# Performance work log

Measured on AMD Instinct MI355X. Metric: run time of the kernel, lower is better.

The kernel has to match this reference:

```python
import jax, jax.numpy as jnp
import numpy as np

EPS = 1e-6
L, H, D, DFF = 4, 6, 6, 64  # n_layers, num_heads(=dim, head_dim=1), d_hid, ffn hidden


def layernorm(x, w, b):
    mu = jnp.mean(x, axis=-1, keepdims=True)
    var = jnp.mean((x - mu) ** 2, axis=-1, keepdims=True)
    return (x - mu) / jnp.sqrt(var + EPS) * w + b


def autocorr(x, qw, qb, kw, kb, vw, vb, l1w, l1b):
    # x: [B,S,H]; head_dim==1 so per-head Linear is scalar w*x+b per head.
    k_in = jnp.concatenate([x[:, :1], x[:, :-1]], axis=1)   # roll right, first row kept
    v_in = jnp.concatenate([x[:, 1:], x[:, -1:]], axis=1)   # roll left, last row kept
    q = x * qw + qb
    k = k_in * kw + kb
    v = v_in * vw + vb
    teo = q * q - k * v                                      # [B,S,H]
    # nn.LayerNorm([1]) over size-1 axis: mean==x, var==0 -> output is bias
    normed = (teo - teo) / jnp.sqrt(EPS) * l1w + l1b
    scores = jax.nn.softmax(normed, axis=1)                  # over seq dim
    return scores * teo


def mha(x, p, li, ai):
    out = autocorr(x, p['qw'][li, ai], p['qb'][li, ai], p['kw'][li, ai],
                   p['kb'][li, ai], p['vw'][li, ai], p['vb'][li, ai],
                   p['ln1_w'][li, ai], p['ln1_b'][li, ai])
    return layernorm(out + x, p['mha_ln_w'][li, ai], p['mha_ln_b'][li, ai])


def setup_inputs() -> dict:
    key = jax.random.key(0)
    ks = jax.random.split(key, 24)
    n = jax.random.normal
    inp = {
        'x_batch': n(ks[0], (128, 4096, 6), jnp.float32),
        'enc_output': n(ks[1], (128, 4096, 6), jnp.float32),
        'dec_ln_w': jnp.ones((D,), jnp.float32),
        'dec_ln_b': jnp.zeros((D,), jnp.float32),
        'qw': n(ks[2], (L, 2, H), jnp.float32),
        'qb': n(ks[3], (L, 2, H), jnp.float32) * 0.1,
        'kw': n(ks[4], (L, 2, H), jnp.float32),
        'kb': n(ks[5], (L, 2, H), jnp.float32) * 0.1,
        'vw': n(ks[6], (L, 2, H), jnp.float32),
        'vb': n(ks[7], (L, 2, H), jnp.float32) * 0.1,
        'ln1_w': jnp.ones((L, 2), jnp.float32),
        'ln1_b': jnp.zeros((L, 2), jnp.float32),
        'mha_ln_w': jnp.ones((L, 2, D), jnp.float32),
        'mha_ln_b': jnp.zeros((L, 2, D), jnp.float32),
        'ffn_w1': n(ks[8], (L, DFF, D), jnp.float32) * (1.0 / np.sqrt(D)),
        'ffn_b1': jnp.zeros((L, DFF), jnp.float32),
        'ffn_w2': n(ks[9], (L, D, DFF), jnp.float32) * (1.0 / np.sqrt(DFF)),
        'ffn_b2': jnp.zeros((L, D), jnp.float32),
        'ffn_ln_w': jnp.ones((L, D), jnp.float32),
        'ffn_ln_b': jnp.zeros((L, D), jnp.float32),
    }
    return inp


def reference(x_batch, enc_output, dec_ln_w, dec_ln_b, qw, qb, kw, kb, vw, vb,
              ln1_w, ln1_b, mha_ln_w, mha_ln_b, ffn_w1, ffn_b1, ffn_w2, ffn_b2,
              ffn_ln_w, ffn_ln_b):
    p = dict(qw=qw, qb=qb, kw=kw, kb=kb, vw=vw, vb=vb, ln1_w=ln1_w, ln1_b=ln1_b,
             mha_ln_w=mha_ln_w, mha_ln_b=mha_ln_b)
    x = layernorm(x_batch, dec_ln_w, dec_ln_b)  # dropout p=0 -> identity
    for li in range(L):
        x = mha(x, p, li, 0)   # self-attention block
        x = mha(x, p, li, 1)   # "enc" attention block (also self, per source)
        h = jax.nn.relu(jnp.einsum('bsd,fd->bsf', x, ffn_w1[li]) + ffn_b1[li])
        y = jnp.einsum('bsf,df->bsd', h, ffn_w2[li]) + ffn_b2[li] + x
        x = layernorm(y, ffn_ln_w[li], ffn_ln_b[li])
    return x
```

## Files before the change

### kernel.cpp

```cpp
#include <hip/hip_runtime.h>

#define S_LEN  4096
#define DM     6
#define NLAYER 4
#define NFF    64
#define HALO   8
#define TPB    256
#define OUT_PER_WAVE 112
#define BLK_X 10

typedef float    vf2 __attribute__((ext_vector_type(2)));
typedef _Float16 vh2 __attribute__((ext_vector_type(2)));

#define REC    13
#define FPAIRS (NFF/2)
#define PACK_TOTAL (NLAYER*FPAIRS*REC)

__device__ __forceinline__ vf2 splat2(float s){ vf2 r; r.x = s; r.y = s; return r; }
__device__ __forceinline__ vh2 bch2(unsigned u){ return __builtin_bit_cast(vh2, u); }

__device__ __forceinline__ unsigned pack2(float lo, float hi){
    _Float16 a = (_Float16)lo, b = (_Float16)hi;
    unsigned short ua = __builtin_bit_cast(unsigned short, a);
    unsigned short ub = __builtin_bit_cast(unsigned short, b);
    return (unsigned)ua | ((unsigned)ub << 16);
}

__global__ void prep_weights(const float* __restrict__ w1,
                             const float* __restrict__ b1,
                             const float* __restrict__ w2,
                             unsigned* __restrict__ ws) {
    int i = blockIdx.x * 256 + threadIdx.x;
    if (i >= PACK_TOTAL) return;
    int li = i / (FPAIRS*REC);
    int r  = i % (FPAIRS*REC);
    int fp = r / REC;
    int j  = r % REC;
    float lo, hi;
    if (j < 6) {
        lo = w1[li*NFF*DM + (2*fp)*DM + j];
        hi = w1[li*NFF*DM + (2*fp+1)*DM + j];
    } else if (j < 12) {
        int d = j - 6;
        lo = w2[li*DM*NFF + d*NFF + 2*fp];
        hi = w2[li*DM*NFF + d*NFF + 2*fp + 1];
    } else {
        lo = b1[li*NFF + 2*fp];
        hi = b1[li*NFF + 2*fp + 1];
    }
    ws[i] = pack2(lo, hi);
}

__device__ __forceinline__ void ln6v(vf2* v, const float* __restrict__ w,
                                     const float* __restrict__ b) {
    vf2 mu = (((v[0]+v[1])+(v[2]+v[3]))+(v[4]+v[5])) * (1.0f/6.0f);
    vf2 var = splat2(0.0f);
#pragma unroll
    for (int d = 0; d < DM; ++d) { vf2 dd = v[d]-mu; var = __builtin_elementwise_fma(dd, dd, var); }
    vf2 a = var * (1.0f/6.0f) + splat2(1e-6f);
    vf2 r; r.x = rsqrtf(a.x); r.y = rsqrtf(a.y);
#pragma unroll
    for (int d = 0; d < DM; ++d)
        v[d] = __builtin_elementwise_fma((v[d]-mu)*r, splat2(w[d]), splat2(b[d]));
}

__global__ __launch_bounds__(TPB)
void decoder_fused(const float* __restrict__ x_batch,
                   const float* __restrict__ dec_ln_w, const float* __restrict__ dec_ln_b,
                   const float* __restrict__ qw, const float* __restrict__ qb,
                   const float* __restrict__ kw, const float* __restrict__ kb,
                   const float* __restrict__ vw, const float* __restrict__ vb,
                   const float* __restrict__ mha_ln_w, const float* __restrict__ mha_ln_b,
                   const unsigned* __restrict__ wsp,
                   const float* __restrict__ ffn_b2,
                   const float* __restrict__ ffn_ln_w, const float* __restrict__ ffn_ln_b,
                   float* __restrict__ out) {
    const int lane = threadIdx.x & 63;
    const int w    = blockIdx.x * (TPB/64) + (threadIdx.x >> 6);
    const int b    = blockIdx.y;
    const int p    = w * OUT_PER_WAVE - HALO + 2*lane;

    vf2 x2[DM];
    if (p >= 0 && p + 1 < S_LEN) {
        const float4* s = reinterpret_cast<const float4*>(x_batch + ((size_t)b*S_LEN + p)*DM);
        float4 a0 = s[0], a1 = s[1], a2 = s[2];
        x2[0].x=a0.x; x2[1].x=a0.y; x2[2].x=a0.z; x2[3].x=a0.w; x2[4].x=a1.x; x2[5].x=a1.y;
        x2[0].y=a1.z; x2[1].y=a1.w; x2[2].y=a2.x; x2[3].y=a2.y; x2[4].y=a2.z; x2[5].y=a2.w;
    } else {
        const int pc = min(max(p, 0), S_LEN-1);
        const float2* s = reinterpret_cast<const float2*>(x_batch + ((size_t)b*S_LEN + pc)*DM);
        float2 a0 = s[0], a1 = s[1], a2 = s[2];
        x2[0] = splat2(a0.x); x2[1] = splat2(a0.y); x2[2] = splat2(a1.x);
        x2[3] = splat2(a1.y); x2[4] = splat2(a2.x); x2[5] = splat2(a2.y);
    }

    ln6v(x2, dec_ln_w, dec_ln_b);

#pragma unroll 1
    for (int li = 0; li < NLAYER; ++li) {
#pragma unroll 1
        for (int ai = 0; ai < 2; ++ai) {
            const int base = (li*2 + ai) * DM;
            vf2 xm[DM], xp[DM];
#pragma unroll
            for (int d = 0; d < DM; ++d) {
                float up = __shfl_up (x2[d].y, 1);
                float dn = __shfl_down(x2[d].x, 1);
                xm[d].x = (p <= 0) ? x2[d].x : up;
                xm[d].y = x2[d].x;
                xp[d].x = x2[d].y;
                xp[d].y = (p + 1 >= S_LEN - 1) ? x2[d].y : dn;
            }
#pragma unroll
            for (int d = 0; d < DM; ++d) {
                vf2 q = __builtin_elementwise_fma(x2[d], splat2(qw[base+d]), splat2(qb[base+d]));
                vf2 k = __builtin_elementwise_fma(xm[d], splat2(kw[base+d]), splat2(kb[base+d]));
                vf2 v = __builtin_elementwise_fma(xp[d], splat2(vw[base+d]), splat2(vb[base+d]));
                vf2 teo = __builtin_elementwise_fma(q, q, -(k*v));
                x2[d] = __builtin_elementwise_fma(teo, splat2(1.0f/(float)S_LEN), x2[d]);
            }
            ln6v(x2, mha_ln_w + base, mha_ln_b + base);
        }

        {
            const unsigned* wl = wsp + (size_t)li * FPAIRS * REC;
            const float*    b2 = ffn_b2 + li*DM;

            vh2 xdA[DM], xdB[DM];
#pragma unroll
            for (int d = 0; d < DM; ++d) {
                _Float16 ha = (_Float16)x2[d].x, hb = (_Float16)x2[d].y;
                xdA[d].x = ha; xdA[d].y = ha;
                xdB[d].x = hb; xdB[d].y = hb;
            }
            vh2 accA[DM], accB[DM];
#pragma unroll
            for (int d = 0; d < DM; ++d) { accA[d] = (vh2)(_Float16)0; accB[d] = (vh2)(_Float16)0; }

#pragma unroll 8
            for (int fp = 0; fp < FPAIRS; ++fp) {
                const unsigned* wp = wl + fp*REC;
                vh2 hA = bch2(wp[12]);
                vh2 hB = hA;
#pragma unroll
                for (int d = 0; d < DM; ++d) {
                    vh2 w1p = bch2(wp[d]);
                    hA = __builtin_elementwise_fma(xdA[d], w1p, hA);
                    hB = __builtin_elementwise_fma(xdB[d], w1p, hB);
                }
                vh2 z = (vh2)(_Float16)0;
                hA = __builtin_elementwise_max(hA, z);
                hB = __builtin_elementwise_max(hB, z);
#pragma unroll
                for (int d = 0; d < DM; ++d) {
                    vh2 w2p = bch2(wp[6+d]);
                    accA[d] = __builtin_elementwise_fma(hA, w2p, accA[d]);
                    accB[d] = __builtin_elementwise_fma(hB, w2p, accB[d]);
                }
            }
#pragma unroll
            for (int d = 0; d < DM; ++d) {
                x2[d].x = x2[d].x + b2[d] + ((float)accA[d].x + (float)accA[d].y);
                x2[d].y = x2[d].y + b2[d] + ((float)accB[d].x + (float)accB[d].y);
            }
            ln6v(x2, ffn_ln_w + li*DM, ffn_ln_b + li*DM);
        }
    }

    if (lane >= 4 && lane < 60 && p < S_LEN) {
        float4* dst = reinterpret_cast<float4*>(out + ((size_t)b*S_LEN + p)*DM);
        float4 a0, a1, a2;
        a0.x=x2[0].x; a0.y=x2[1].x; a0.z=x2[2].x; a0.w=x2[3].x;
        a1.x=x2[4].x; a1.y=x2[5].x; a1.z=x2[0].y; a1.w=x2[1].y;
        a2.x=x2[2].y; a2.y=x2[3].y; a2.z=x2[4].y; a2.w=x2[5].y;
        dst[0]=a0; dst[1]=a1; dst[2]=a2;
    }
}

extern "C" void kernel_launch(void* const* d_in, const int* in_sizes, int n_in,
                              void* d_out, int out_size, void* d_ws, size_t ws_size,
                              hipStream_t stream) {
    const float* x_batch  = (const float*)d_in[0];
    const float* dec_ln_w = (const float*)d_in[2];
    const float* dec_ln_b = (const float*)d_in[3];
    const float* qw       = (const float*)d_in[4];
    const float* qb       = (const float*)d_in[5];
    const float* kw       = (const float*)d_in[6];
    const float* kb       = (const float*)d_in[7];
    const float* vw       = (const float*)d_in[8];
    const float* vb       = (const float*)d_in[9];
    const float* mha_ln_w = (const float*)d_in[12];
    const float* mha_ln_b = (const float*)d_in[13];
    const float* ffn_w1   = (const float*)d_in[14];
    const float* ffn_b1   = (const float*)d_in[15];
    const float* ffn_w2   = (const float*)d_in[16];
    const float* ffn_b2   = (const float*)d_in[17];
    const float* ffn_ln_w = (const float*)d_in[18];
    const float* ffn_ln_b = (const float*)d_in[19];
    float* out = (float*)d_out;
    unsigned* wsp = (unsigned*)d_ws;

    prep_weights<<<(PACK_TOTAL + 255)/256, 256, 0, stream>>>(ffn_w1, ffn_b1, ffn_w2, wsp);

    const int B = in_sizes[0] / (S_LEN * DM);
    dim3 grid(BLK_X, B);
    decoder_fused<<<grid, TPB, 0, stream>>>(
        x_batch, dec_ln_w, dec_ln_b, qw, qb, kw, kb, vw, vb,
        mha_ln_w, mha_ln_b, wsp, ffn_b2, ffn_ln_w, ffn_ln_b, out);
}
```

Baseline: 155.2 us.

## Compute FFN with MFMA 16x16x16 f16 via per-wave LDS staging

```diff
diff --git a/kernel.cpp b/kernel.cpp
--- a/kernel.cpp
+++ b/kernel.cpp
@@ -10,15 +10,24 @@
 #define BLK_X 10
 
 typedef float    vf2 __attribute__((ext_vector_type(2)));
+typedef float    vf4 __attribute__((ext_vector_type(4)));
 typedef _Float16 vh2 __attribute__((ext_vector_type(2)));
-
-#define REC    13
-#define FPAIRS (NFF/2)
-#define PACK_TOTAL (NLAYER*FPAIRS*REC)
+typedef _Float16 vh4 __attribute__((ext_vector_type(4)));
+
+#define W1A_OFF 0
+#define W2A_OFF 2048
+#define PACK_TOTAL 4096
+
+#define XSTRIDE 40
+#define XSZ (128*XSTRIDE)
+#define YSTRIDE 132
+#define YSZ (8*YSTRIDE*4)
+#define WAVE_LDS (XSZ + YSZ)
 
 __device__ __forceinline__ vf2 splat2(float s){ vf2 r; r.x = s; r.y = s; return r; }
-__device__ __forceinline__ vh2 bch2(unsigned u){ return __builtin_bit_cast(vh2, u); }
-
+__device__ __forceinline__ unsigned pkh(float a, float b){
+    return __builtin_bit_cast(unsigned, __builtin_amdgcn_cvt_pkrtz(a, b));
+}
 __device__ __forceinline__ unsigned pack2(float lo, float hi){
     _Float16 a = (_Float16)lo, b = (_Float16)hi;
     unsigned short ua = __builtin_bit_cast(unsigned short, a);
@@ -26,27 +35,30 @@
     return (unsigned)ua | ((unsigned)ub << 16);
 }
 
-__global__ void prep_weights(const float* __restrict__ w1,
-                             const float* __restrict__ b1,
-                             const float* __restrict__ w2,
-                             unsigned* __restrict__ ws) {
+__global__ void prep_frags(const float* __restrict__ w1,
+                           const float* __restrict__ w2,
+                           unsigned* __restrict__ ws) {
     int i = blockIdx.x * 256 + threadIdx.x;
     if (i >= PACK_TOTAL) return;
-    int li = i / (FPAIRS*REC);
-    int r  = i % (FPAIRS*REC);
-    int fp = r / REC;
-    int j  = r % REC;
-    float lo, hi;
-    if (j < 6) {
-        lo = w1[li*NFF*DM + (2*fp)*DM + j];
-        hi = w1[li*NFF*DM + (2*fp+1)*DM + j];
-    } else if (j < 12) {
-        int d = j - 6;
-        lo = w2[li*DM*NFF + d*NFF + 2*fp];
-        hi = w2[li*DM*NFF + d*NFF + 2*fp + 1];
+    int which = i >> 11;
+    int r  = i & 2047;
+    int li = r >> 9;
+    int q  = r & 511;
+    int tile = q >> 7;
+    int rem  = q & 127;
+    int lane = rem >> 1;
+    int dwj  = rem & 1;
+    int c = lane & 15, g = lane >> 4;
+    float lo = 0.f, hi = 0.f;
+    if (which == 0) {
+        int f  = tile*16 + c;
+        int d0 = g*4 + 2*dwj;
+        if (d0   < DM) lo = w1[li*NFF*DM + f*DM + d0];
+        if (d0+1 < DM) hi = w1[li*NFF*DM + f*DM + d0+1];
     } else {
-        lo = b1[li*NFF + 2*fp];
-        hi = b1[li*NFF + 2*fp + 1];
+        int d = c;
+        int f = tile*16 + g*4 + 2*dwj;
+        if (d < DM) { lo = w2[li*DM*NFF + d*NFF + f]; hi = w2[li*DM*NFF + d*NFF + f+1]; }
     }
     ws[i] = pack2(lo, hi);
 }
@@ -72,13 +84,26 @@
                    const float* __restrict__ vw, const float* __restrict__ vb,
                    const float* __restrict__ mha_ln_w, const float* __restrict__ mha_ln_b,
                    const unsigned* __restrict__ wsp,
-                   const float* __restrict__ ffn_b2,
+                   const float* __restrict__ ffn_b1, const float* __restrict__ ffn_b2,
                    const float* __restrict__ ffn_ln_w, const float* __restrict__ ffn_ln_b,
                    float* __restrict__ out) {
     const int lane = threadIdx.x & 63;
-    const int w    = blockIdx.x * (TPB/64) + (threadIdx.x >> 6);
+    const int wid  = threadIdx.x >> 6;
+    const int w    = blockIdx.x * (TPB/64) + wid;
     const int b    = blockIdx.y;
     const int p    = w * OUT_PER_WAVE - HALO + 2*lane;
+    const int c    = lane & 15, g = lane >> 4;
+
+    __shared__ __align__(16) char smem[(TPB/64) * WAVE_LDS];
+    char* wbase = smem + wid * WAVE_LDS;
+    char* Xb = wbase;
+    char* Yb = wbase + XSZ;
+
+    {
+        uint4 z = make_uint4(0,0,0,0);
+#pragma unroll
+        for (int i = 0; i < 5; ++i) *(uint4*)(wbase + lane*80 + i*16) = z;
+    }
 
     vf2 x2[DM];
     if (p >= 0 && p + 1 < S_LEN) {
@@ -98,6 +123,18 @@
 
 #pragma unroll 1
     for (int li = 0; li < NLAYER; ++li) {
+        vh4 w1f[4], w2f[4]; vf4 b1f[4];
+#pragma unroll
+        for (int mt = 0; mt < 4; ++mt) {
+            uint2 u = *((const uint2*)wsp + (li*4 + mt)*64 + lane);
+            w1f[mt] = __builtin_bit_cast(vh4, u);
+            uint2 v = *((const uint2*)wsp + (W2A_OFF/2) + (li*4 + mt)*64 + lane);
+            w2f[mt] = __builtin_bit_cast(vh4, v);
+            float4 bb = *reinterpret_cast<const float4*>(ffn_b1 + li*NFF + mt*16 + g*4);
+            vf4 bv; bv.x=bb.x; bv.y=bb.y; bv.z=bb.z; bv.w=bb.w;
+            b1f[mt] = bv;
+        }
+
 #pragma unroll 1
         for (int ai = 0; ai < 2; ++ai) {
             const int base = (li*2 + ai) * DM;
@@ -123,45 +160,49 @@
         }
 
         {
-            const unsigned* wl = wsp + (size_t)li * FPAIRS * REC;
-            const float*    b2 = ffn_b2 + li*DM;
-
-            vh2 xdA[DM], xdB[DM];
+            {
+                unsigned d0 = pkh(x2[0].x,x2[1].x), d1 = pkh(x2[2].x,x2[3].x), d2 = pkh(x2[4].x,x2[5].x);
+                unsigned e0 = pkh(x2[0].y,x2[1].y), e1 = pkh(x2[2].y,x2[3].y), e2 = pkh(x2[4].y,x2[5].y);
+                char* r0 = Xb + (2*lane)*XSTRIDE;
+                *(uint2*)r0 = make_uint2(d0,d1); *(unsigned*)(r0+8) = d2;
+                char* r1 = r0 + XSTRIDE;
+                *(uint2*)r1 = make_uint2(e0,e1); *(unsigned*)(r1+8) = e2;
+            }
+            vh4 bfrag[8];
+#pragma unroll
+            for (int t = 0; t < 8; ++t)
+                bfrag[t] = *(const vh4*)(Xb + (16*t + c)*XSTRIDE + g*8);
+
+#pragma unroll
+            for (int t = 0; t < 8; ++t) {
+                vh4 hb[4];
+#pragma unroll
+                for (int ft = 0; ft < 4; ++ft) {
+                    vf4 hc = __builtin_amdgcn_mfma_f32_16x16x16f16(w1f[ft], bfrag[t], b1f[ft], 0, 0, 0);
+                    unsigned lo = pkh(fmaxf(hc.x,0.f), fmaxf(hc.y,0.f));
+                    unsigned hi = pkh(fmaxf(hc.z,0.f), fmaxf(hc.w,0.f));
+                    uint2 u = make_uint2(lo, hi);
+                    hb[ft] = __builtin_bit_cast(vh4, u);
+                }
+                vf4 yacc; yacc.x=0.f; yacc.y=0.f; yacc.z=0.f; yacc.w=0.f;
+#pragma unroll
+                for (int ks = 0; ks < 4; ++ks)
+                    yacc = __builtin_amdgcn_mfma_f32_16x16x16f16(w2f[ks], hb[ks], yacc, 0, 0, 0);
+                if (lane < 32) {
+                    int col = 16*t + c;
+                    float* yp = (float*)Yb;
+                    yp[(g*4+0)*YSTRIDE + col] = yacc.x;
+                    yp[(g*4+1)*YSTRIDE + col] = yacc.y;
+                    yp[(g*4+2)*YSTRIDE + col] = yacc.z;
+                    yp[(g*4+3)*YSTRIDE + col] = yacc.w;
+                }
+            }
+            const float* b2 = ffn_b2 + li*DM;
 #pragma unroll
             for (int d = 0; d < DM; ++d) {
-                _Float16 ha = (_Float16)x2[d].x, hb = (_Float16)x2[d].y;
-                xdA[d].x = ha; xdA[d].y = ha;
-                xdB[d].x = hb; xdB[d].y = hb;
-            }
-            vh2 accA[DM], accB[DM];
-#pragma unroll
-            for (int d = 0; d < DM; ++d) { accA[d] = (vh2)(_Float16)0; accB[d] = (vh2)(_Float16)0; }
-
-#pragma unroll 8
-            for (int fp = 0; fp < FPAIRS; ++fp) {
-                const unsigned* wp = wl + fp*REC;
-                vh2 hA = bch2(wp[12]);
-                vh2 hB = hA;
-#pragma unroll
-                for (int d = 0; d < DM; ++d) {
-                    vh2 w1p = bch2(wp[d]);
-                    hA = __builtin_elementwise_fma(xdA[d], w1p, hA);
-                    hB = __builtin_elementwise_fma(xdB[d], w1p, hB);
-                }
-                vh2 z = (vh2)(_Float16)0;
-                hA = __builtin_elementwise_max(hA, z);
-                hB = __builtin_elementwise_max(hB, z);
-#pragma unroll
-                for (int d = 0; d < DM; ++d) {
-                    vh2 w2p = bch2(wp[6+d]);
-                    accA[d] = __builtin_elementwise_fma(hA, w2p, accA[d]);
-                    accB[d] = __builtin_elementwise_fma(hB, w2p, accB[d]);
-                }
-            }
-#pragma unroll
-            for (int d = 0; d < DM; ++d) {
-                x2[d].x = x2[d].x + b2[d] + ((float)accA[d].x + (float)accA[d].y);
-                x2[d].y = x2[d].y + b2[d] + ((float)accB[d].x + (float)accB[d].y);
+                float2 yv = *(const float2*)((float*)Yb + d*YSTRIDE + 2*lane);
+                vf2 t2; t2.x = yv.x; t2.y = yv.y;
+                x2[d] = x2[d] + splat2(b2[d]) + t2;
             }
             ln6v(x2, ffn_ln_w + li*DM, ffn_ln_b + li*DM);
         }
@@ -200,11 +241,11 @@
     float* out = (float*)d_out;
     unsigned* wsp = (unsigned*)d_ws;
 
-    prep_weights<<<(PACK_TOTAL + 255)/256, 256, 0, stream>>>(ffn_w1, ffn_b1, ffn_w2, wsp);
+    prep_frags<<<(PACK_TOTAL + 255)/256, 256, 0, stream>>>(ffn_w1, ffn_w2, wsp);
 
     const int B = in_sizes[0] / (S_LEN * DM);
     dim3 grid(BLK_X, B);
     decoder_fused<<<grid, TPB, 0, stream>>>(
         x_batch, dec_ln_w, dec_ln_b, qw, qb, kw, kb, vw, vb,
-        mha_ln_w, mha_ln_b, wsp, ffn_b2, ffn_ln_w, ffn_ln_b, out);
-}
+        mha_ln_w, mha_ln_b, wsp, ffn_b1, ffn_b2, ffn_ln_w, ffn_ln_b, out);
+}
```

Result: faster. 140.8 us (-9.3%).
